# Kernel tuning notes

Hardware: AMD Instinct MI355X
Metric: run time of the kernel (lower is better)

Reference implementation:

```python
import jax, jax.numpy as jnp
import numpy as np


def _binarize(x):
    # tf.where(x < 0, -1.0, 1.0)
    return jnp.where(x < 0, -1.0, 1.0).astype(jnp.float32)


def setup_inputs() -> dict:
    key = jax.random.key(0)
    k1, k2, k3 = jax.random.split(key, 3)
    M, K, N = 8192, 2048, 2048
    inputs = jax.random.normal(k1, (M, K), dtype=jnp.float32)
    kernel = jax.random.normal(k2, (K, N), dtype=jnp.float32) * 0.1
    bias = jax.random.normal(k3, (N,), dtype=jnp.float32) * 0.01
    return {"inputs": inputs, "kernel": kernel, "bias": bias}


def reference(inputs, kernel, bias):
    bx = _binarize(inputs)          # [M, K] in {-1, +1}
    bw = _binarize(kernel)          # [K, N] in {-1, +1}
    return jnp.matmul(bx, bw) + bias  # [M, N]
```

## Files before the change

### kernel.cpp

```cpp
#include <hip/hip_runtime.h>
#include <stdint.h>

typedef __attribute__((ext_vector_type(4))) int int4v;
typedef __attribute__((ext_vector_type(8))) int int8v;
typedef __attribute__((ext_vector_type(4))) float floatx4;
typedef __attribute__((ext_vector_type(16))) unsigned char uchar16;

#define MDIM 8192
#define KDIM 2048
#define NDIM 2048
#define BM 128
#define BN 128
#define KB 1024
#define BKB 128

__device__ __forceinline__ void load16_lds(const void* g, void* l) {
  __builtin_amdgcn_global_load_lds(
      (const __attribute__((address_space(1))) void*)g,
      (__attribute__((address_space(3))) void*)l, 16, 0, 0);
}

#define XBLK 2048
#define WBLK 512

__global__ void binarize_fused(const float* __restrict__ X,
                               const float* __restrict__ W,
                               unsigned char* __restrict__ Xb,
                               unsigned char* __restrict__ WbT) {
  const int b = blockIdx.x;
  if (b < XBLK) {
    size_t i = ((size_t)b * 256 + threadIdx.x) * 32;
    const float4* xp = (const float4*)(X + i);
    uchar16 o;
#pragma unroll
    for (int h = 0; h < 8; ++h) {
      float4 a = xp[h];
      unsigned n0 = (a.x < 0.f) ? 0xAu : 0x2u;
      unsigned n1 = (a.y < 0.f) ? 0xAu : 0x2u;
      unsigned n2 = (a.z < 0.f) ? 0xAu : 0x2u;
      unsigned n3 = (a.w < 0.f) ? 0xAu : 0x2u;
      o[2 * h]     = (unsigned char)(n0 | (n1 << 4));
      o[2 * h + 1] = (unsigned char)(n2 | (n3 << 4));
    }
    *(uchar16*)(Xb + i / 2) = o;
  } else {
    const int bw = b - XBLK;
    const int nb = bw & 31;
    const int kb = bw >> 5;
    const int nn = threadIdx.x & 63;
    const int kc = kb * 4 + (threadIdx.x >> 6);
    const float* wp = W + (size_t)(kc * 32) * NDIM + nb * 64 + nn;
    uchar16 o;
#pragma unroll
    for (int j = 0; j < 16; ++j) {
      unsigned lo = (wp[(size_t)(2 * j) * NDIM] < 0.f) ? 0xAu : 0x2u;
      unsigned hi = (wp[(size_t)(2 * j + 1) * NDIM] < 0.f) ? 0xAu : 0x2u;
      o[j] = (unsigned char)(lo | (hi << 4));
    }
    *(uchar16*)(WbT + (size_t)(nb * 64 + nn) * KB + kc * 16) = o;
  }
}

__global__ __launch_bounds__(256) void gemm_bin_fp4(
    const unsigned char* __restrict__ A,
    const unsigned char* __restrict__ B,
    const float* __restrict__ bias,
    float* __restrict__ C) {
  __shared__ __align__(16) unsigned char As[BM * BKB];
  __shared__ __align__(16) unsigned char Bs[BN * BKB];

  const int tid = threadIdx.x;
  const int lane = tid & 63;
  const int wv = tid >> 6;
  const int wm = wv >> 1;
  const int wn = wv & 1;
  const int r = lane & 15;
  const int q = lane >> 4;

  const int m0 = blockIdx.x * BM;
  const int n0 = blockIdx.y * BN;

  floatx4 acc[4][4] = {};

  const int qbase = wv * 256;

  int srcoff[4];
#pragma unroll
  for (int i = 0; i < 4; ++i) {
    const int s = qbase + i * 64 + lane;
    const int row = s >> 3;
    const int cg = (s & 7) ^ (row & 7);
    srcoff[i] = row * KB + cg * 16;
  }
  const unsigned char* Ab = A + (size_t)m0 * KB;
  const unsigned char* Bb = B + (size_t)n0 * KB;

  for (int kb = 0; kb < KB; kb += BKB) {
#pragma unroll
    for (int i = 0; i < 4; ++i) {
      load16_lds(Ab + kb + srcoff[i], As + (qbase + i * 64) * 16);
      load16_lds(Bb + kb + srcoff[i], Bs + (qbase + i * 64) * 16);
    }
    __syncthreads();

#pragma unroll
    for (int s2 = 0; s2 < 2; ++s2) {
      const int cswz = ((s2 * 4 + q) ^ (r & 7)) * 16;
      int8v b8[4];
#pragma unroll
      for (int tn = 0; tn < 4; ++tn) {
        int4v bv = *(const int4v*)(Bs + (wn * 64 + tn * 16 + r) * BKB + cswz);
        b8[tn] = int8v{bv[0], bv[1], bv[2], bv[3], 0, 0, 0, 0};
      }
#pragma unroll
      for (int tm = 0; tm < 4; ++tm) {
        int4v av = *(const int4v*)(As + (wm * 64 + tm * 16 + r) * BKB + cswz);
        int8v a8 = int8v{av[0], av[1], av[2], av[3], 0, 0, 0, 0};
#pragma unroll
        for (int tn = 0; tn < 4; ++tn)
          acc[tm][tn] = __builtin_amdgcn_mfma_scale_f32_16x16x128_f8f6f4(
              a8, b8[tn], acc[tm][tn], 4, 4,
              0, 0x7F7F7F7F, 0, 0x7F7F7F7F);
      }
    }
    __syncthreads();
  }

  float* slab = (float*)(&As[0]) + wv * 1024;

  float bv[4];
#pragma unroll
  for (int tn = 0; tn < 4; ++tn) bv[tn] = bias[n0 + wn * 64 + tn * 16 + r];

  const int lrow = lane >> 4;
  const int lc4 = lane & 15;

#pragma unroll
  for (int tm = 0; tm < 4; ++tm) {
#pragma unroll
    for (int tn = 0; tn < 4; ++tn)
#pragma unroll
      for (int v = 0; v < 4; ++v)
        slab[(q * 4 + v) * 64 + tn * 16 + r] = acc[tm][tn][v] + bv[tn];
    asm volatile("s_waitcnt lgkmcnt(0)" ::: "memory");
    __builtin_amdgcn_sched_barrier(0);
#pragma unroll
    for (int j = 0; j < 4; ++j) {
      const int row = j * 4 + lrow;
      floatx4 val = *(const floatx4*)(&slab[row * 64 + lc4 * 4]);
      *(floatx4*)(&C[(size_t)(m0 + wm * 64 + tm * 16 + row) * NDIM +
                     n0 + wn * 64 + lc4 * 4]) = val;
    }
    asm volatile("s_waitcnt lgkmcnt(0)" ::: "memory");
    __builtin_amdgcn_sched_barrier(0);
  }
}

extern "C" void kernel_launch(void* const* d_in, const int* in_sizes, int n_in,
                              void* d_out, int out_size, void* d_ws, size_t ws_size,
                              hipStream_t stream) {
  const float* X = (const float*)d_in[0];
  const float* W = (const float*)d_in[1];
  const float* bias = (const float*)d_in[2];
  float* out = (float*)d_out;

  unsigned char* Xb = (unsigned char*)d_ws;
  unsigned char* WbT = Xb + (size_t)MDIM * KDIM / 2;

  binarize_fused<<<dim3(XBLK + WBLK), 256, 0, stream>>>(X, W, Xb, WbT);
  gemm_bin_fp4<<<dim3(MDIM / BM, NDIM / BN), 256, 0, stream>>>(Xb, WbT, bias, out);
}
```

Measured before the change: 145.3 us.

## Compute two N-tiles per block and overlap first tile's epilogue with second GEMM

Each block now uses 512 threads with a 256x256 output region, computed as two sequential 256x128 sub-GEMMs sharing the A tile stream. While the second sub-GEMM runs its K-loop, the first sub-GEMM's accumulators are written out in half-chunks through a dedicated LDS slab. Next-k loads are issued before each epilogue chunk and waited on with vmcnt. The aim is to hide the output-store epilogue behind MFMA work and double the tile size per block. The cost is twice the accumulator registers per thread, which puts pressure on occupancy, and A is reloaded for the second pass.

Result: slower. 148.6 us (+2.3%).

```diff
diff --git a/kernel.cpp b/kernel.cpp
--- a/kernel.cpp
+++ b/kernel.cpp
@@ -9,10 +9,11 @@
 #define MDIM 8192
 #define KDIM 2048
 #define NDIM 2048
-#define BM 128
+#define BM 256
 #define BN 128
 #define KB 1024
 #define BKB 128
+#define NKT 8
 
 __device__ __forceinline__ void load16_lds(const void* g, void* l) {
   __builtin_amdgcn_global_load_lds(
@@ -61,13 +62,59 @@
   }
 }
 
-__global__ __launch_bounds__(256) void gemm_bin_fp4(
+__device__ __forceinline__ void kstep(const unsigned char* As_, const unsigned char* Bs_,
+                                      floatx4 (&acc)[4][4], int wm, int wn, int r, int q) {
+#pragma unroll
+  for (int s2 = 0; s2 < 2; ++s2) {
+    const int cswz = ((s2 * 4 + q) ^ (r & 7)) * 16;
+    int8v b8[4];
+#pragma unroll
+    for (int tn = 0; tn < 4; ++tn) {
+      int4v bv = *(const int4v*)(Bs_ + (wn * 64 + tn * 16 + r) * BKB + cswz);
+      b8[tn] = int8v{bv[0], bv[1], bv[2], bv[3], 0, 0, 0, 0};
+    }
+#pragma unroll
+    for (int tm = 0; tm < 4; ++tm) {
+      int4v av = *(const int4v*)(As_ + (wm * 64 + tm * 16 + r) * BKB + cswz);
+      int8v a8 = int8v{av[0], av[1], av[2], av[3], 0, 0, 0, 0};
+#pragma unroll
+      for (int tn = 0; tn < 4; ++tn)
+        acc[tm][tn] = __builtin_amdgcn_mfma_scale_f32_16x16x128_f8f6f4(
+            a8, b8[tn], acc[tm][tn], 4, 4, 0, 0x7F7F7F7F, 0, 0x7F7F7F7F);
+    }
+  }
+}
+
+__device__ __forceinline__ void half_chunk(float* slab, const floatx4 (&acc)[4][4],
+                                           int tm, int tnh, const float* bv,
+                                           float* __restrict__ C, int m0, int wm,
+                                           int ncolbase, int lane, int r, int q) {
+#pragma unroll
+  for (int tn2 = 0; tn2 < 2; ++tn2) {
+    const int tn = tnh * 2 + tn2;
+#pragma unroll
+    for (int v = 0; v < 4; ++v)
+      slab[(q * 4 + v) * 32 + tn2 * 16 + r] = acc[tm][tn][v] + bv[tn];
+  }
+  asm volatile("s_waitcnt lgkmcnt(0)" ::: "memory");
+  __builtin_amdgcn_sched_barrier(0);
+  const int rr = lane >> 3, c4 = lane & 7;
+#pragma unroll
+  for (int h = 0; h < 2; ++h) {
+    const int row = h * 8 + rr;
+    floatx4 val = *(const floatx4*)(&slab[row * 32 + c4 * 4]);
+    *(floatx4*)(&C[(size_t)(m0 + wm * 64 + tm * 16 + row) * NDIM + ncolbase + c4 * 4]) = val;
+  }
+}
+
+__global__ __launch_bounds__(512, 2) void gemm_bin_fp4(
     const unsigned char* __restrict__ A,
     const unsigned char* __restrict__ B,
     const float* __restrict__ bias,
     float* __restrict__ C) {
   __shared__ __align__(16) unsigned char As[BM * BKB];
   __shared__ __align__(16) unsigned char Bs[BN * BKB];
+  __shared__ __align__(16) float Sl[8 * 512];
 
   const int tid = threadIdx.x;
   const int lane = tid & 63;
@@ -78,82 +125,89 @@
   const int q = lane >> 4;
 
   const int m0 = blockIdx.x * BM;
-  const int n0 = blockIdx.y * BN;
-
-  floatx4 acc[4][4] = {};
-
-  const int qbase = wv * 256;
-
-  int srcoff[4];
+  const int n0 = blockIdx.y * 256;
+
+  floatx4 acc1[4][4] = {};
+  floatx4 acc2[4][4] = {};
+
+  int srcA[4], srcB[2];
 #pragma unroll
   for (int i = 0; i < 4; ++i) {
-    const int s = qbase + i * 64 + lane;
+    const int s = wv * 256 + i * 64 + lane;
     const int row = s >> 3;
-    const int cg = (s & 7) ^ (row & 7);
-    srcoff[i] = row * KB + cg * 16;
+    srcA[i] = row * KB + (((s & 7) ^ (row & 7)) * 16);
+  }
+#pragma unroll
+  for (int i = 0; i < 2; ++i) {
+    const int s = wv * 128 + i * 64 + lane;
+    const int row = s >> 3;
+    srcB[i] = row * KB + (((s & 7) ^ (row & 7)) * 16);
   }
   const unsigned char* Ab = A + (size_t)m0 * KB;
-  const unsigned char* Bb = B + (size_t)n0 * KB;
-
-  for (int kb = 0; kb < KB; kb += BKB) {
-#pragma unroll
-    for (int i = 0; i < 4; ++i) {
-      load16_lds(Ab + kb + srcoff[i], As + (qbase + i * 64) * 16);
-      load16_lds(Bb + kb + srcoff[i], Bs + (qbase + i * 64) * 16);
-    }
+  const unsigned char* Bb1 = B + (size_t)n0 * KB;
+  const unsigned char* Bb2 = B + (size_t)(n0 + BN) * KB;
+
+  float* slab = Sl + wv * 512;
+
+  for (int t = 0; t < NKT; ++t) {
+    const int kb = t * BKB;
+#pragma unroll
+    for (int i = 0; i < 4; ++i)
+      load16_lds(Ab + kb + srcA[i], As + (wv * 256 + i * 64) * 16);
+#pragma unroll
+    for (int i = 0; i < 2; ++i)
+      load16_lds(Bb1 + kb + srcB[i], Bs + (wv * 128 + i * 64) * 16);
     __syncthreads();
-
-#pragma unroll
-    for (int s2 = 0; s2 < 2; ++s2) {
-      const int cswz = ((s2 * 4 + q) ^ (r & 7)) * 16;
-      int8v b8[4];
-#pragma unroll
-      for (int tn = 0; tn < 4; ++tn) {
-        int4v bv = *(const int4v*)(Bs + (wn * 64 + tn * 16 + r) * BKB + cswz);
-        b8[tn] = int8v{bv[0], bv[1], bv[2], bv[3], 0, 0, 0, 0};
-      }
-#pragma unroll
-      for (int tm = 0; tm < 4; ++tm) {
-        int4v av = *(const int4v*)(As + (wm * 64 + tm * 16 + r) * BKB + cswz);
-        int8v a8 = int8v{av[0], av[1], av[2], av[3], 0, 0, 0, 0};
-#pragma unroll
-        for (int tn = 0; tn < 4; ++tn)
-          acc[tm][tn] = __builtin_amdgcn_mfma_scale_f32_16x16x128_f8f6f4(
-              a8, b8[tn], acc[tm][tn], 4, 4,
-              0, 0x7F7F7F7F, 0, 0x7F7F7F7F);
-      }
-    }
+    kstep(As, Bs, acc1, wm, wn, r, q);
     __syncthreads();
   }
 
-  float* slab = (float*)(&As[0]) + wv * 1024;
-
-  float bv[4];
-#pragma unroll
-  for (int tn = 0; tn < 4; ++tn) bv[tn] = bias[n0 + wn * 64 + tn * 16 + r];
-
-  const int lrow = lane >> 4;
-  const int lc4 = lane & 15;
-
-#pragma unroll
-  for (int tm = 0; tm < 4; ++tm) {
-#pragma unroll
-    for (int tn = 0; tn < 4; ++tn)
-#pragma unroll
-      for (int v = 0; v < 4; ++v)
-        slab[(q * 4 + v) * 64 + tn * 16 + r] = acc[tm][tn][v] + bv[tn];
+  float bv1[4];
+#pragma unroll
+  for (int tn = 0; tn < 4; ++tn) bv1[tn] = bias[n0 + wn * 64 + tn * 16 + r];
+
+#pragma unroll
+  for (int i = 0; i < 4; ++i)
+    load16_lds(Ab + srcA[i], As + (wv * 256 + i * 64) * 16);
+#pragma unroll
+  for (int i = 0; i < 2; ++i)
+    load16_lds(Bb2 + srcB[i], Bs + (wv * 128 + i * 64) * 16);
+
+#pragma unroll
+  for (int t = 0; t < NKT; ++t) {
+    if (t == 0) asm volatile("s_waitcnt vmcnt(0)" ::: "memory");
+    else        asm volatile("s_waitcnt vmcnt(2)" ::: "memory");
+    __builtin_amdgcn_s_barrier();
+    __builtin_amdgcn_sched_barrier(0);
+    kstep(As, Bs, acc2, wm, wn, r, q);
     asm volatile("s_waitcnt lgkmcnt(0)" ::: "memory");
+    __builtin_amdgcn_s_barrier();
     __builtin_amdgcn_sched_barrier(0);
-#pragma unroll
-    for (int j = 0; j < 4; ++j) {
-      const int row = j * 4 + lrow;
-      floatx4 val = *(const floatx4*)(&slab[row * 64 + lc4 * 4]);
-      *(floatx4*)(&C[(size_t)(m0 + wm * 64 + tm * 16 + row) * NDIM +
-                     n0 + wn * 64 + lc4 * 4]) = val;
-    }
-    asm volatile("s_waitcnt lgkmcnt(0)" ::: "memory");
-    __builtin_amdgcn_sched_barrier(0);
-  }
+    if (t < NKT - 1) {
+      const int kb = (t + 1) * BKB;
+#pragma unroll
+      for (int i = 0; i < 4; ++i)
+        load16_lds(Ab + kb + srcA[i], As + (wv * 256 + i * 64) * 16);
+#pragma unroll
+      for (int i = 0; i < 2; ++i)
+        load16_lds(Bb2 + kb + srcB[i], Bs + (wv * 128 + i * 64) * 16);
+    }
+    half_chunk(slab, acc1, t >> 1, t & 1, bv1, C, m0, wm,
+               n0 + wn * 64 + (t & 1) * 32, lane, r, q);
+  }
+
+  float bv2[4];
+#pragma unroll
+  for (int tn = 0; tn < 4; ++tn) bv2[tn] = bias[n0 + BN + wn * 64 + tn * 16 + r];
+#pragma unroll
+  for (int tm = 0; tm < 4; ++tm)
+#pragma unroll
+    for (int tnh = 0; tnh < 2; ++tnh) {
+      half_chunk(slab, acc2, tm, tnh, bv2, C, m0, wm,
+                 n0 + BN + wn * 64 + tnh * 32, lane, r, q);
+      asm volatile("s_waitcnt lgkmcnt(0)" ::: "memory");
+      __builtin_amdgcn_sched_barrier(0);
+    }
 }
 
 extern "C" void kernel_launch(void* const* d_in, const int* in_sizes, int n_in,
@@ -168,5 +222,5 @@
   unsigned char* WbT = Xb + (size_t)MDIM * KDIM / 2;
 
   binarize_fused<<<dim3(XBLK + WBLK), 256, 0, stream>>>(X, W, Xb, WbT);
-  gemm_bin_fp4<<<dim3(MDIM / BM, NDIM / BN), 256, 0, stream>>>(Xb, WbT, bias, out);
-}
+  gemm_bin_fp4<<<dim3(MDIM / BM, NDIM / 256), 512, 0, stream>>>(Xb, WbT, bias, out);
+}
```
